# Kernel tuning notes

Measured on AMD Instinct MI355X. Metric: run time of the kernel, lower is better.

## Reference

```python
import jax, jax.numpy as jnp
import numpy as np

B, L, D = 128, 196, 1024  # batch, att_size, rnn_size


def setup_inputs() -> dict:
    key = jax.random.key(0)
    ks = jax.random.split(key, 11)
    s = 1.0 / np.sqrt(D)
    return {
        "x": jax.random.normal(ks[0], (B, D), jnp.float32),
        "att": jax.random.normal(ks[1], (B, L, D), jnp.float32),
        "h": jax.random.normal(ks[2], (B, D), jnp.float32),
        "W_a2a": jax.random.uniform(ks[3], (D, D), jnp.float32, -s, s),
        "b_a2a": jax.random.uniform(ks[4], (D,), jnp.float32, -s, s),
        "W_h2a": jax.random.uniform(ks[5], (D, D), jnp.float32, -s, s),
        "b_h2a": jax.random.uniform(ks[6], (D,), jnp.float32, -s, s),
        "W_i2a": jax.random.uniform(ks[7], (D, D), jnp.float32, -s, s),
        "b_i2a": jax.random.uniform(ks[8], (D,), jnp.float32, -s, s),
        "W_d2d": jax.random.uniform(ks[9], (D,), jnp.float32, -s, s),
        "b_d2d": jax.random.uniform(ks[10], (), jnp.float32, -s, s),
    }


def reference(x, att, h, W_a2a, b_a2a, W_h2a, b_h2a, W_i2a, b_i2a, W_d2d, b_d2d):
    # att_v_1: [B, L, D]
    att_v = jnp.einsum('bld,ed->ble', att, W_a2a) + b_a2a
    att_h = (h @ W_h2a.T + b_h2a)[:, None, :]   # [B, 1, D]
    att_x = (x @ W_i2a.T + b_i2a)[:, None, :]   # [B, 1, D]
    dot = jnp.tanh(att_v + att_h + att_x)       # [B, L, D]
    scores = jnp.einsum('bld,d->bl', dot, W_d2d) + b_d2d  # [B, L]
    weight = jax.nn.softmax(scores, axis=-1)    # [B, L]
    att_res = jnp.einsum('bld,bl->bd', att, weight)  # [B, D]
    return att_res
```

## Files before the change

kernel.cpp:

```cpp
#include <hip/hip_runtime.h>
#include <hip/hip_bf16.h>

#define B_ 128
#define L_ 196
#define D_ 1024

typedef __attribute__((ext_vector_type(8))) short short8v;
typedef __attribute__((ext_vector_type(4))) float f32x4;
typedef unsigned short ushort_t;

#define OFF_ATTBF   0UL
#define OFF_WBF     51380224UL
#define OFF_A2      53477376UL
#define OFF_W2      54001664UL
#define OFF_SPART   53477376UL
#define OFF_CPART   58195968UL

__device__ inline unsigned short f2bf(float f) {
  unsigned int u = __float_as_uint(f);
  unsigned int r = (u + 0x7fffu + ((u >> 16) & 1u)) >> 16;
  return (unsigned short)r;
}

__global__ void convert_kernel(const float* __restrict__ att, const float* __restrict__ Wa,
                               const float* __restrict__ x,   const float* __restrict__ h,
                               const float* __restrict__ Wi,  const float* __restrict__ Wh,
                               ushort_t* __restrict__ att_bf, ushort_t* __restrict__ W_bf,
                               ushort_t* __restrict__ A2,     ushort_t* __restrict__ W2) {
  const int n0 = (B_*L_*D_)/4;
  const int n1 = (D_*D_)/4;
  const int n2 = (B_*D_)/4;
  const int total = n0 + n1 + 2*n2 + 2*n1;
  for (int idx = blockIdx.x*blockDim.x + threadIdx.x; idx < total;
       idx += gridDim.x*blockDim.x) {
    const float4* src; ushort_t* dst;
    int i = idx;
    if (i < n0)               { src = (const float4*)att + i; dst = att_bf + (size_t)i*4; }
    else if ((i -= n0) < n1)  { src = (const float4*)Wa  + i; dst = W_bf  + (size_t)i*4; }
    else if ((i -= n1) < n2)  { int b = i>>8, k4 = i&255; src = (const float4*)x  + i; dst = A2 + b*2048 + k4*4; }
    else if ((i -= n2) < n2)  { int b = i>>8, k4 = i&255; src = (const float4*)h  + i; dst = A2 + b*2048 + 1024 + k4*4; }
    else if ((i -= n2) < n1)  { int e = i>>8, k4 = i&255; src = (const float4*)Wi + i; dst = W2 + e*2048 + k4*4; }
    else { i -= n1;             int e = i>>8, k4 = i&255; src = (const float4*)Wh + i; dst = W2 + e*2048 + 1024 + k4*4; }
    float4 v = *src;
    ushort4 o; o.x = f2bf(v.x); o.y = f2bf(v.y); o.z = f2bf(v.z); o.w = f2bf(v.w);
    *(ushort4*)dst = o;
  }
}

__device__ inline void stage_tile(const ushort_t* __restrict__ g, int row0, int Kld, int k0,
                                  ushort_t* ldst, int t) {
  #pragma unroll
  for (int it = 0; it < 4; ++it) {
    int linear = it*4096 + t*16;
    int r = linear >> 7;
    int c = (t & 7) ^ (r & 7);
    const ushort_t* src = g + (size_t)(row0 + r)*Kld + k0 + c*8;
    ushort_t* dst = ldst + ((it*4096 + ((t & 192) << 4)) >> 1);
    __builtin_amdgcn_global_load_lds((const __attribute__((address_space(1))) void*)src,
                                     (__attribute__((address_space(3))) void*)dst,
                                     16, 0, 0);
  }
}

__device__ inline short8v ldfrag(const ushort_t* tile, int row, int c) {
  int phys = c ^ (row & 7);
  return *(const short8v*)(tile + row*64 + phys*8);
}

__global__ __launch_bounds__(256) void gemm_c_kernel(
    const ushort_t* __restrict__ Amat, const ushort_t* __restrict__ Bmat,
    float* __restrict__ cpart) {
  __shared__ ushort_t lds[32768];
  int bid = blockIdx.x;
  int e0 = (bid & 7)*128;
  int kc = bid >> 3;
  int kbeg = kc*512;
  const int Kld = 2048;
  int t = threadIdx.x, lane = t & 63, w = t >> 6;
  int wm = w >> 1, we = w & 1;
  int lrow = lane & 15;
  int lk = lane >> 4;

  f32x4 acc[4][4];
  #pragma unroll
  for (int i = 0; i < 4; ++i)
    #pragma unroll
    for (int j = 0; j < 4; ++j) acc[i][j] = (f32x4){0.f, 0.f, 0.f, 0.f};

  stage_tile(Amat, 0,  Kld, kbeg, lds, t);
  stage_tile(Bmat, e0, Kld, kbeg, lds + 8192, t);
  __syncthreads();

  const int nk = 8;
  for (int kt = 0; kt < nk; ++kt) {
    int cur = kt & 1;
    if (kt + 1 < nk) {
      stage_tile(Amat, 0,  Kld, kbeg + ((kt+1) << 6), lds + (cur^1)*16384, t);
      stage_tile(Bmat, e0, Kld, kbeg + ((kt+1) << 6), lds + (cur^1)*16384 + 8192, t);
    }
    const ushort_t* At = lds + cur*16384;
    const ushort_t* Bt = At + 8192;
    #pragma unroll
    for (int hh = 0; hh < 2; ++hh) {
      short8v af[4], bfv[4];
      #pragma unroll
      for (int i = 0; i < 4; ++i) af[i]  = ldfrag(At, wm*64 + i*16 + lrow, hh*4 + lk);
      #pragma unroll
      for (int j = 0; j < 4; ++j) bfv[j] = ldfrag(Bt, we*64 + j*16 + lrow, hh*4 + lk);
      #pragma unroll
      for (int i = 0; i < 4; ++i)
        #pragma unroll
        for (int j = 0; j < 4; ++j)
          acc[i][j] = __builtin_amdgcn_mfma_f32_16x16x32_bf16(af[i], bfv[j], acc[i][j], 0, 0, 0);
    }
    __syncthreads();
  }

  float* outc = cpart + (size_t)kc*131072;
  #pragma unroll
  for (int i = 0; i < 4; ++i) {
    int m = wm*64 + i*16 + lk*4;
    #pragma unroll
    for (int j = 0; j < 4; ++j) {
      int e = e0 + we*64 + j*16 + lrow;
      #pragma unroll
      for (int r = 0; r < 4; ++r)
        outc[(m + r)*1024 + e] = acc[i][j][r];
    }
  }
}

#define BARR()  __builtin_amdgcn_s_barrier()
#define VM0()   asm volatile("s_waitcnt vmcnt(0)" ::: "memory")

__device__ inline void stageS(const ushort_t* __restrict__ g, int k0, ushort_t* ldsbase, int t) {
  #pragma unroll
  for (int it = 0; it < 4; ++it) {
    int linear = it*4096 + t*16;
    int r = linear >> 7;
    int c = ((linear >> 4) & 7) ^ (r & 7);
    const ushort_t* src = g + (size_t)r*1024 + k0 + c*8;
    ushort_t* dst = ldsbase + ((it*4096 + ((t & 192) << 4)) >> 1);
    __builtin_amdgcn_global_load_lds((const __attribute__((address_space(1))) void*)src,
                                     (__attribute__((address_space(3))) void*)dst,
                                     16, 0, 0);
  }
}

__global__ __launch_bounds__(256) void gemm_score_kernel(
    const ushort_t* __restrict__ Amat, const ushort_t* __restrict__ Bmat,
    const float* __restrict__ cpart,
    const float* __restrict__ ba, const float* __restrict__ bh, const float* __restrict__ bi,
    const float* __restrict__ wd,
    float* __restrict__ spart) {
  __shared__ ushort_t lds[16384];
  __shared__ float c_lds[256];
  int bid = blockIdx.x;
  int swz = (bid & 7)*196 + (bid >> 3);
  int m_blk = swz >> 3, n_blk = swz & 7;
  int m0 = m_blk*128, e0 = n_blk*128;
  int t = (int)threadIdx.x, lane = t & 63, w = t >> 6;
  int wm = w >> 1, we = w & 1;
  int lrow = lane & 15, lk = lane >> 4;

  int bb0 = m0 / 196;
  {
    int bb = bb0 + (t >> 7);
    int e  = e0 + (t & 127);
    float v = ba[e] + bh[e] + bi[e];
    if (bb < 128) {
      v += cpart[bb*1024 + e] + cpart[131072 + bb*1024 + e]
         + cpart[262144 + bb*1024 + e] + cpart[393216 + bb*1024 + e];
    }
    c_lds[t] = v;
  }

  const ushort_t* aG = Amat + (size_t)m0*1024;
  const ushort_t* bG = Bmat + (size_t)e0*1024;

  int lrow7 = lrow & 7;
  const ushort_t* pA0 = lds + (wm*64 + lrow)*64 + ((lk)     ^ lrow7)*8;
  const ushort_t* pA1 = lds + (wm*64 + lrow)*64 + (((4+lk)) ^ lrow7)*8;
  const ushort_t* pB0 = lds + 8192 + (we*64 + lrow)*64 + ((lk)     ^ lrow7)*8;
  const ushort_t* pB1 = lds + 8192 + (we*64 + lrow)*64 + (((4+lk)) ^ lrow7)*8;

  f32x4 acc[4][4];
  #pragma unroll
  for (int i = 0; i < 4; ++i)
    #pragma unroll
    for (int j = 0; j < 4; ++j) acc[i][j] = (f32x4){0.f, 0.f, 0.f, 0.f};

  stageS(aG, 0, lds, t);
  stageS(bG, 0, lds + 8192, t);

  for (int kt = 0; kt < 16; ++kt) {
    VM0();
    BARR();
    __builtin_amdgcn_s_setprio(1);
    #pragma unroll
    for (int ks = 0; ks < 2; ++ks) {
      const ushort_t* pa = ks ? pA1 : pA0;
      const ushort_t* pb = ks ? pB1 : pB0;
      short8v af[4], bfv[4];
      #pragma unroll
      for (int i = 0; i < 4; ++i) af[i]  = *(const short8v*)(pa + i*1024);
      #pragma unroll
      for (int j = 0; j < 4; ++j) bfv[j] = *(const short8v*)(pb + j*1024);
      #pragma unroll
      for (int i = 0; i < 4; ++i)
        #pragma unroll
        for (int j = 0; j < 4; ++j)
          acc[i][j] = __builtin_amdgcn_mfma_f32_16x16x32_bf16(af[i], bfv[j], acc[i][j], 0, 0, 0);
    }
    __builtin_amdgcn_s_setprio(0);
    BARR();
    if (kt < 15) {
      stageS(aG, (kt+1)*64, lds, t);
      stageS(bG, (kt+1)*64, lds + 8192, t);
    }
  }

  int p = n_blk*2 + we;
  #pragma unroll
  for (int i = 0; i < 4; ++i) {
    int mbase = m0 + wm*64 + i*16 + lk*4;
    f32x4 ps;
    #pragma unroll
    for (int r = 0; r < 4; ++r) {
      int m = mbase + r;
      int bb = (int)((unsigned)m / 196u);
      float partial = 0.f;
      #pragma unroll
      for (int j = 0; j < 4; ++j) {
        int ee = we*64 + j*16 + lrow;
        float v = acc[i][j][r] + c_lds[(bb - bb0)*128 + ee];
        float ex = __expf(2.f*v);
        partial += (1.f - 2.f/(ex + 1.f)) * wd[e0 + ee];
      }
      partial += __shfl_xor(partial, 1);
      partial += __shfl_xor(partial, 2);
      partial += __shfl_xor(partial, 4);
      partial += __shfl_xor(partial, 8);
      ps[r] = partial;
    }
    if (lrow == 0) *(f32x4*)(spart + (size_t)p*25088 + mbase) = ps;
  }
}

__global__ __launch_bounds__(256) void finalize_kernel(const ushort_t* __restrict__ att_bf,
                                                       const float* __restrict__ spart,
                                                       float* __restrict__ out) {
  int b  = blockIdx.x >> 1;
  int dh = blockIdx.x & 1;
  int t  = threadIdx.x;
  __shared__ float wls[L_];
  __shared__ float red[8];

  float s = -1e30f;
  if (t < L_) {
    int m = b*L_ + t;
    float sum = 0.f;
    #pragma unroll
    for (int p = 0; p < 16; ++p) sum += spart[p*25088 + m];
    s = sum;
  }
  float mx = s;
  #pragma unroll
  for (int off = 1; off < 64; off <<= 1) mx = fmaxf(mx, __shfl_xor(mx, off));
  if ((t & 63) == 0) red[t >> 6] = mx;
  __syncthreads();
  mx = fmaxf(fmaxf(red[0], red[1]), fmaxf(red[2], red[3]));
  float pr = (t < L_) ? __expf(s - mx) : 0.f;
  float ssum = pr;
  #pragma unroll
  for (int off = 1; off < 64; off <<= 1) ssum += __shfl_xor(ssum, off);
  if ((t & 63) == 0) red[4 + (t >> 6)] = ssum;
  __syncthreads();
  float tot = red[4] + red[5] + red[6] + red[7];
  if (t < L_) wls[t] = pr / tot;
  __syncthreads();

  int d = dh*512 + t*2;
  const ushort_t* abase = att_bf + (size_t)b*L_*D_ + d;
  float a0 = 0.f, a1 = 0.f;
  #pragma unroll 4
  for (int l = 0; l < L_; ++l) {
    float wv = wls[l];
    unsigned int v = *(const unsigned int*)(abase + (size_t)l*D_);
    float lo = __uint_as_float(v << 16);
    float hi = __uint_as_float(v & 0xffff0000u);
    a0 += wv*lo; a1 += wv*hi;
  }
  float2 o; o.x = a0; o.y = a1;
  *(float2*)(out + (size_t)b*D_ + d) = o;
}

extern "C" void kernel_launch(void* const* d_in, const int* in_sizes, int n_in,
                              void* d_out, int out_size, void* d_ws, size_t ws_size,
                              hipStream_t stream) {
  (void)in_sizes; (void)n_in; (void)out_size; (void)ws_size;
  const float* x   = (const float*)d_in[0];
  const float* att = (const float*)d_in[1];
  const float* h   = (const float*)d_in[2];
  const float* Wa  = (const float*)d_in[3];
  const float* ba  = (const float*)d_in[4];
  const float* Wh  = (const float*)d_in[5];
  const float* bh  = (const float*)d_in[6];
  const float* Wi  = (const float*)d_in[7];
  const float* bi  = (const float*)d_in[8];
  const float* wd  = (const float*)d_in[9];

  char* ws = (char*)d_ws;
  ushort_t* att_bf = (ushort_t*)(ws + OFF_ATTBF);
  ushort_t* W_bf   = (ushort_t*)(ws + OFF_WBF);
  ushort_t* A2     = (ushort_t*)(ws + OFF_A2);
  ushort_t* W2     = (ushort_t*)(ws + OFF_W2);
  float*    cpart  = (float*)(ws + OFF_CPART);
  float*    spart  = (float*)(ws + OFF_SPART);
  float*    out    = (float*)d_out;

  hipLaunchKernelGGL(convert_kernel, dim3(2048), dim3(256), 0, stream,
                     att, Wa, x, h, Wi, Wh, att_bf, W_bf, A2, W2);
  hipLaunchKernelGGL(gemm_c_kernel, dim3(32), dim3(256), 0, stream,
                     A2, W2, cpart);
  hipLaunchKernelGGL(gemm_score_kernel, dim3(1568), dim3(256), 0, stream,
                     att_bf, W_bf, cpart, ba, bh, bi, wd, spart);
  hipLaunchKernelGGL(finalize_kernel, dim3(256), dim3(256), 0, stream,
                     att_bf, spart, out);
}
```

Baseline: 127.7 us.

## Switch score GEMM to 32x32x16 MFMA and split finalize over more blocks

Replaces the 16x16x32 bf16 MFMA tiling in the score GEMM with 32x32x16 MFMAs on 2x2 accumulator tiles per wave. This cuts LDS fragment loads per MFMA and uses the larger instruction, and the tanh/score epilogue is remapped to the 32x32 output layout with a wider shuffle reduction. Separately, the finalize kernel now uses four blocks per batch with 128 active threads each, adding parallelism in the weighted-sum phase but leaving half the threads idle and recomputing the softmax twice as often. The new epilogue does scalar stores per row instead of vector stores.

```diff
diff --git a/kernel.cpp b/kernel.cpp
--- a/kernel.cpp
+++ b/kernel.cpp
@@ -7,6 +7,7 @@
 
 typedef __attribute__((ext_vector_type(8))) short short8v;
 typedef __attribute__((ext_vector_type(4))) float f32x4;
+typedef __attribute__((ext_vector_type(16))) float f32x16;
 typedef unsigned short ushort_t;
 
 #define OFF_ATTBF   0UL
@@ -161,7 +162,7 @@
   int m0 = m_blk*128, e0 = n_blk*128;
   int t = (int)threadIdx.x, lane = t & 63, w = t >> 6;
   int wm = w >> 1, we = w & 1;
-  int lrow = lane & 15, lk = lane >> 4;
+  int l31 = lane & 31, hi = lane >> 5, l7 = lane & 7;
 
   int bb0 = m0 / 196;
   {
@@ -178,17 +179,18 @@
   const ushort_t* aG = Amat + (size_t)m0*1024;
   const ushort_t* bG = Bmat + (size_t)e0*1024;
 
-  int lrow7 = lrow & 7;
-  const ushort_t* pA0 = lds + (wm*64 + lrow)*64 + ((lk)     ^ lrow7)*8;
-  const ushort_t* pA1 = lds + (wm*64 + lrow)*64 + (((4+lk)) ^ lrow7)*8;
-  const ushort_t* pB0 = lds + 8192 + (we*64 + lrow)*64 + ((lk)     ^ lrow7)*8;
-  const ushort_t* pB1 = lds + 8192 + (we*64 + lrow)*64 + (((4+lk)) ^ lrow7)*8;
-
-  f32x4 acc[4][4];
-  #pragma unroll
-  for (int i = 0; i < 4; ++i)
-    #pragma unroll
-    for (int j = 0; j < 4; ++j) acc[i][j] = (f32x4){0.f, 0.f, 0.f, 0.f};
+  const ushort_t* pA0 = lds + (wm*64 + l31)*64;
+  const ushort_t* pA1 = pA0 + 2048;
+  const ushort_t* pB0 = lds + 8192 + (we*64 + l31)*64;
+  const ushort_t* pB1 = pB0 + 2048;
+
+  f32x16 acc[2][2];
+  #pragma unroll
+  for (int i = 0; i < 2; ++i)
+    #pragma unroll
+    for (int j = 0; j < 2; ++j)
+      #pragma unroll
+      for (int r = 0; r < 16; ++r) acc[i][j][r] = 0.f;
 
   stageS(aG, 0, lds, t);
   stageS(bG, 0, lds + 8192, t);
@@ -198,19 +200,16 @@
     BARR();
     __builtin_amdgcn_s_setprio(1);
     #pragma unroll
-    for (int ks = 0; ks < 2; ++ks) {
-      const ushort_t* pa = ks ? pA1 : pA0;
-      const ushort_t* pb = ks ? pB1 : pB0;
-      short8v af[4], bfv[4];
-      #pragma unroll
-      for (int i = 0; i < 4; ++i) af[i]  = *(const short8v*)(pa + i*1024);
-      #pragma unroll
-      for (int j = 0; j < 4; ++j) bfv[j] = *(const short8v*)(pb + j*1024);
-      #pragma unroll
-      for (int i = 0; i < 4; ++i)
-        #pragma unroll
-        for (int j = 0; j < 4; ++j)
-          acc[i][j] = __builtin_amdgcn_mfma_f32_16x16x32_bf16(af[i], bfv[j], acc[i][j], 0, 0, 0);
+    for (int ks = 0; ks < 4; ++ks) {
+      int off = (((ks*2 + hi) ^ l7) * 8);
+      short8v a0 = *(const short8v*)(pA0 + off);
+      short8v a1 = *(const short8v*)(pA1 + off);
+      short8v b0 = *(const short8v*)(pB0 + off);
+      short8v b1 = *(const short8v*)(pB1 + off);
+      acc[0][0] = __builtin_amdgcn_mfma_f32_32x32x16_bf16(a0, b0, acc[0][0], 0, 0, 0);
+      acc[0][1] = __builtin_amdgcn_mfma_f32_32x32x16_bf16(a0, b1, acc[0][1], 0, 0, 0);
+      acc[1][0] = __builtin_amdgcn_mfma_f32_32x32x16_bf16(a1, b0, acc[1][0], 0, 0, 0);
+      acc[1][1] = __builtin_amdgcn_mfma_f32_32x32x16_bf16(a1, b1, acc[1][1], 0, 0, 0);
     }
     __builtin_amdgcn_s_setprio(0);
     BARR();
@@ -222,36 +221,34 @@
 
   int p = n_blk*2 + we;
   #pragma unroll
-  for (int i = 0; i < 4; ++i) {
-    int mbase = m0 + wm*64 + i*16 + lk*4;
-    f32x4 ps;
-    #pragma unroll
-    for (int r = 0; r < 4; ++r) {
-      int m = mbase + r;
+  for (int i = 0; i < 2; ++i) {
+    #pragma unroll
+    for (int reg = 0; reg < 16; ++reg) {
+      int m = m0 + wm*64 + i*32 + (reg&3) + 8*(reg>>2) + 4*hi;
       int bb = (int)((unsigned)m / 196u);
-      float partial = 0.f;
-      #pragma unroll
-      for (int j = 0; j < 4; ++j) {
-        int ee = we*64 + j*16 + lrow;
-        float v = acc[i][j][r] + c_lds[(bb - bb0)*128 + ee];
+      float s = 0.f;
+      #pragma unroll
+      for (int j = 0; j < 2; ++j) {
+        int ee = we*64 + j*32 + l31;
+        float v = acc[i][j][reg] + c_lds[(bb - bb0)*128 + ee];
         float ex = __expf(2.f*v);
-        partial += (1.f - 2.f/(ex + 1.f)) * wd[e0 + ee];
+        s += (1.f - 2.f/(ex + 1.f)) * wd[e0 + ee];
       }
-      partial += __shfl_xor(partial, 1);
-      partial += __shfl_xor(partial, 2);
-      partial += __shfl_xor(partial, 4);
-      partial += __shfl_xor(partial, 8);
-      ps[r] = partial;
-    }
-    if (lrow == 0) *(f32x4*)(spart + (size_t)p*25088 + mbase) = ps;
+      s += __shfl_xor(s, 1);
+      s += __shfl_xor(s, 2);
+      s += __shfl_xor(s, 4);
+      s += __shfl_xor(s, 8);
+      s += __shfl_xor(s, 16);
+      if (l31 == 0) spart[(size_t)p*25088 + m] = s;
+    }
   }
 }
 
 __global__ __launch_bounds__(256) void finalize_kernel(const ushort_t* __restrict__ att_bf,
                                                        const float* __restrict__ spart,
                                                        float* __restrict__ out) {
-  int b  = blockIdx.x >> 1;
-  int dh = blockIdx.x & 1;
+  int b  = blockIdx.x >> 2;
+  int dq = blockIdx.x & 3;
   int t  = threadIdx.x;
   __shared__ float wls[L_];
   __shared__ float red[8];
@@ -280,19 +277,21 @@
   if (t < L_) wls[t] = pr / tot;
   __syncthreads();
 
-  int d = dh*512 + t*2;
-  const ushort_t* abase = att_bf + (size_t)b*L_*D_ + d;
-  float a0 = 0.f, a1 = 0.f;
-  #pragma unroll 4
-  for (int l = 0; l < L_; ++l) {
-    float wv = wls[l];
-    unsigned int v = *(const unsigned int*)(abase + (size_t)l*D_);
-    float lo = __uint_as_float(v << 16);
-    float hi = __uint_as_float(v & 0xffff0000u);
-    a0 += wv*lo; a1 += wv*hi;
-  }
-  float2 o; o.x = a0; o.y = a1;
-  *(float2*)(out + (size_t)b*D_ + d) = o;
+  if (t < 128) {
+    int d = dq*256 + t*2;
+    const ushort_t* abase = att_bf + (size_t)b*L_*D_ + d;
+    float a0 = 0.f, a1 = 0.f;
+    #pragma unroll 4
+    for (int l = 0; l < L_; ++l) {
+      float wv = wls[l];
+      unsigned int v = *(const unsigned int*)(abase + (size_t)l*D_);
+      float lo = __uint_as_float(v << 16);
+      float hif = __uint_as_float(v & 0xffff0000u);
+      a0 += wv*lo; a1 += wv*hif;
+    }
+    float2 o; o.x = a0; o.y = a1;
+    *(float2*)(out + (size_t)b*D_ + d) = o;
+  }
 }
 
 extern "C" void kernel_launch(void* const* d_in, const int* in_sizes, int n_in,
@@ -325,6 +324,6 @@
                      A2, W2, cpart);
   hipLaunchKernelGGL(gemm_score_kernel, dim3(1568), dim3(256), 0, stream,
                      att_bf, W_bf, cpart, ba, bh, bi, wd, spart);
-  hipLaunchKernelGGL(finalize_kernel, dim3(256), dim3(256), 0, stream,
+  hipLaunchKernelGGL(finalize_kernel, dim3(512), dim3(256), 0, stream,
                      att_bf, spart, out);
 }
```

Measured after the change: 148.8 us. 1.17x slower.

## Make score GEMM persistent with next-tile prefetch; split finalize over quarters

Applied to the files above, without the earlier changes.

The score GEMM now runs as a persistent grid of 768 blocks, each looping over the 1568 tiles. The first K-slice of the next tile is prefetched during the last K-step of the current one, which hides part of the per-tile prologue latency. The finalize kernel is split into four D-quarters per batch row instead of two, giving more blocks for the bandwidth-bound weighted sum. The cost is that only half the threads in each finalize block do the sum, and the softmax work is repeated in every block. With a 768-block grid, tiles are spread unevenly: some blocks get three tiles and others two, which adds tail imbalance.

```diff
diff --git a/kernel.cpp b/kernel.cpp
--- a/kernel.cpp
+++ b/kernel.cpp
@@ -155,28 +155,10 @@
     float* __restrict__ spart) {
   __shared__ ushort_t lds[16384];
   __shared__ float c_lds[256];
-  int bid = blockIdx.x;
-  int swz = (bid & 7)*196 + (bid >> 3);
-  int m_blk = swz >> 3, n_blk = swz & 7;
-  int m0 = m_blk*128, e0 = n_blk*128;
+  const int NT = 1568, GRID = 768;
   int t = (int)threadIdx.x, lane = t & 63, w = t >> 6;
   int wm = w >> 1, we = w & 1;
   int lrow = lane & 15, lk = lane >> 4;
-
-  int bb0 = m0 / 196;
-  {
-    int bb = bb0 + (t >> 7);
-    int e  = e0 + (t & 127);
-    float v = ba[e] + bh[e] + bi[e];
-    if (bb < 128) {
-      v += cpart[bb*1024 + e] + cpart[131072 + bb*1024 + e]
-         + cpart[262144 + bb*1024 + e] + cpart[393216 + bb*1024 + e];
-    }
-    c_lds[t] = v;
-  }
-
-  const ushort_t* aG = Amat + (size_t)m0*1024;
-  const ushort_t* bG = Bmat + (size_t)e0*1024;
 
   int lrow7 = lrow & 7;
   const ushort_t* pA0 = lds + (wm*64 + lrow)*64 + ((lk)     ^ lrow7)*8;
@@ -184,74 +166,105 @@
   const ushort_t* pB0 = lds + 8192 + (we*64 + lrow)*64 + ((lk)     ^ lrow7)*8;
   const ushort_t* pB1 = lds + 8192 + (we*64 + lrow)*64 + (((4+lk)) ^ lrow7)*8;
 
-  f32x4 acc[4][4];
-  #pragma unroll
-  for (int i = 0; i < 4; ++i)
-    #pragma unroll
-    for (int j = 0; j < 4; ++j) acc[i][j] = (f32x4){0.f, 0.f, 0.f, 0.f};
-
-  stageS(aG, 0, lds, t);
-  stageS(bG, 0, lds + 8192, t);
-
-  for (int kt = 0; kt < 16; ++kt) {
-    VM0();
-    BARR();
-    __builtin_amdgcn_s_setprio(1);
-    #pragma unroll
-    for (int ks = 0; ks < 2; ++ks) {
-      const ushort_t* pa = ks ? pA1 : pA0;
-      const ushort_t* pb = ks ? pB1 : pB0;
-      short8v af[4], bfv[4];
-      #pragma unroll
-      for (int i = 0; i < 4; ++i) af[i]  = *(const short8v*)(pa + i*1024);
-      #pragma unroll
-      for (int j = 0; j < 4; ++j) bfv[j] = *(const short8v*)(pb + j*1024);
-      #pragma unroll
-      for (int i = 0; i < 4; ++i)
-        #pragma unroll
-        for (int j = 0; j < 4; ++j)
-          acc[i][j] = __builtin_amdgcn_mfma_f32_16x16x32_bf16(af[i], bfv[j], acc[i][j], 0, 0, 0);
-    }
-    __builtin_amdgcn_s_setprio(0);
-    BARR();
-    if (kt < 15) {
-      stageS(aG, (kt+1)*64, lds, t);
-      stageS(bG, (kt+1)*64, lds + 8192, t);
-    }
-  }
-
-  int p = n_blk*2 + we;
-  #pragma unroll
-  for (int i = 0; i < 4; ++i) {
-    int mbase = m0 + wm*64 + i*16 + lk*4;
-    f32x4 ps;
-    #pragma unroll
-    for (int r = 0; r < 4; ++r) {
-      int m = mbase + r;
-      int bb = (int)((unsigned)m / 196u);
-      float partial = 0.f;
-      #pragma unroll
-      for (int j = 0; j < 4; ++j) {
-        int ee = we*64 + j*16 + lrow;
-        float v = acc[i][j][r] + c_lds[(bb - bb0)*128 + ee];
-        float ex = __expf(2.f*v);
-        partial += (1.f - 2.f/(ex + 1.f)) * wd[e0 + ee];
+  {
+    int tid0 = blockIdx.x;
+    int swz0 = (tid0 & 7)*196 + (tid0 >> 3);
+    stageS(Amat + (size_t)(swz0 >> 3)*131072, 0, lds, t);
+    stageS(Bmat + (size_t)(swz0 & 7)*131072, 0, lds + 8192, t);
+  }
+
+  for (int tid = blockIdx.x; tid < NT; tid += GRID) {
+    int swz = (tid & 7)*196 + (tid >> 3);
+    int m_blk = swz >> 3, n_blk = swz & 7;
+    int m0 = m_blk*128, e0 = n_blk*128;
+    int bb0 = m0 / 196;
+
+    __syncthreads();
+    {
+      int bb = bb0 + (t >> 7);
+      int e  = e0 + (t & 127);
+      float v = ba[e] + bh[e] + bi[e];
+      if (bb < 128) {
+        v += cpart[bb*1024 + e] + cpart[131072 + bb*1024 + e]
+           + cpart[262144 + bb*1024 + e] + cpart[393216 + bb*1024 + e];
       }
-      partial += __shfl_xor(partial, 1);
-      partial += __shfl_xor(partial, 2);
-      partial += __shfl_xor(partial, 4);
-      partial += __shfl_xor(partial, 8);
-      ps[r] = partial;
-    }
-    if (lrow == 0) *(f32x4*)(spart + (size_t)p*25088 + mbase) = ps;
+      c_lds[t] = v;
+    }
+
+    const ushort_t* aG = Amat + (size_t)m0*1024;
+    const ushort_t* bG = Bmat + (size_t)e0*1024;
+
+    f32x4 acc[4][4];
+    #pragma unroll
+    for (int i = 0; i < 4; ++i)
+      #pragma unroll
+      for (int j = 0; j < 4; ++j) acc[i][j] = (f32x4){0.f, 0.f, 0.f, 0.f};
+
+    for (int kt = 0; kt < 16; ++kt) {
+      VM0();
+      BARR();
+      __builtin_amdgcn_s_setprio(1);
+      #pragma unroll
+      for (int ks = 0; ks < 2; ++ks) {
+        const ushort_t* pa = ks ? pA1 : pA0;
+        const ushort_t* pb = ks ? pB1 : pB0;
+        short8v af[4], bfv[4];
+        #pragma unroll
+        for (int i = 0; i < 4; ++i) af[i]  = *(const short8v*)(pa + i*1024);
+        #pragma unroll
+        for (int j = 0; j < 4; ++j) bfv[j] = *(const short8v*)(pb + j*1024);
+        #pragma unroll
+        for (int i = 0; i < 4; ++i)
+          #pragma unroll
+          for (int j = 0; j < 4; ++j)
+            acc[i][j] = __builtin_amdgcn_mfma_f32_16x16x32_bf16(af[i], bfv[j], acc[i][j], 0, 0, 0);
+      }
+      __builtin_amdgcn_s_setprio(0);
+      BARR();
+      if (kt < 15) {
+        stageS(aG, (kt+1)*64, lds, t);
+        stageS(bG, (kt+1)*64, lds + 8192, t);
+      } else if (tid + GRID < NT) {
+        int nt2 = tid + GRID;
+        int sz2 = (nt2 & 7)*196 + (nt2 >> 3);
+        stageS(Amat + (size_t)(sz2 >> 3)*131072, 0, lds, t);
+        stageS(Bmat + (size_t)(sz2 & 7)*131072, 0, lds + 8192, t);
+      }
+    }
+
+    int p = n_blk*2 + we;
+    #pragma unroll
+    for (int i = 0; i < 4; ++i) {
+      int mbase = m0 + wm*64 + i*16 + lk*4;
+      f32x4 ps;
+      #pragma unroll
+      for (int r = 0; r < 4; ++r) {
+        int m = mbase + r;
+        int bb = (int)((unsigned)m / 196u);
+        float partial = 0.f;
+        #pragma unroll
+        for (int j = 0; j < 4; ++j) {
+          int ee = we*64 + j*16 + lrow;
+          float v = acc[i][j][r] + c_lds[(bb - bb0)*128 + ee];
+          float ex = __expf(2.f*v);
+          partial += (1.f - 2.f/(ex + 1.f)) * wd[e0 + ee];
+        }
+        partial += __shfl_xor(partial, 1);
+        partial += __shfl_xor(partial, 2);
+        partial += __shfl_xor(partial, 4);
+        partial += __shfl_xor(partial, 8);
+        ps[r] = partial;
+      }
+      if (lrow == 0) *(f32x4*)(spart + (size_t)p*25088 + mbase) = ps;
+    }
   }
 }
 
 __global__ __launch_bounds__(256) void finalize_kernel(const ushort_t* __restrict__ att_bf,
                                                        const float* __restrict__ spart,
                                                        float* __restrict__ out) {
-  int b  = blockIdx.x >> 1;
-  int dh = blockIdx.x & 1;
+  int b  = blockIdx.x >> 2;
+  int dq = blockIdx.x & 3;
   int t  = threadIdx.x;
   __shared__ float wls[L_];
   __shared__ float red[8];
@@ -280,19 +293,21 @@
   if (t < L_) wls[t] = pr / tot;
   __syncthreads();
 
-  int d = dh*512 + t*2;
-  const ushort_t* abase = att_bf + (size_t)b*L_*D_ + d;
-  float a0 = 0.f, a1 = 0.f;
-  #pragma unroll 4
-  for (int l = 0; l < L_; ++l) {
-    float wv = wls[l];
-    unsigned int v = *(const unsigned int*)(abase + (size_t)l*D_);
-    float lo = __uint_as_float(v << 16);
-    float hi = __uint_as_float(v & 0xffff0000u);
-    a0 += wv*lo; a1 += wv*hi;
-  }
-  float2 o; o.x = a0; o.y = a1;
-  *(float2*)(out + (size_t)b*D_ + d) = o;
+  if (t < 128) {
+    int d = dq*256 + t*2;
+    const ushort_t* abase = att_bf + (size_t)b*L_*D_ + d;
+    float a0 = 0.f, a1 = 0.f;
+    #pragma unroll 4
+    for (int l = 0; l < L_; ++l) {
+      float wv = wls[l];
+      unsigned int v = *(const unsigned int*)(abase + (size_t)l*D_);
+      float lo = __uint_as_float(v << 16);
+      float hif = __uint_as_float(v & 0xffff0000u);
+      a0 += wv*lo; a1 += wv*hif;
+    }
+    float2 o; o.x = a0; o.y = a1;
+    *(float2*)(out + (size_t)b*D_ + d) = o;
+  }
 }
 
 extern "C" void kernel_launch(void* const* d_in, const int* in_sizes, int n_in,
@@ -323,8 +338,8 @@
                      att, Wa, x, h, Wi, Wh, att_bf, W_bf, A2, W2);
   hipLaunchKernelGGL(gemm_c_kernel, dim3(32), dim3(256), 0, stream,
                      A2, W2, cpart);
-  hipLaunchKernelGGL(gemm_score_kernel, dim3(1568), dim3(256), 0, stream,
+  hipLaunchKernelGGL(gemm_score_kernel, dim3(768), dim3(256), 0, stream,
                      att_bf, W_bf, cpart, ba, bh, bi, wd, spart);
-  hipLaunchKernelGGL(finalize_kernel, dim3(256), dim3(256), 0, stream,
+  hipLaunchKernelGGL(finalize_kernel, dim3(512), dim3(256), 0, stream,
                      att_bf, spart, out);
 }
```

Result: slower. 149.4 us (+17.0%).

## Fuse att fp32-to-bf16 conversion into GEMM A-tile load path

Applied to the files above, without the earlier changes.

Removes the separate pass that converts the whole att tensor to bf16 in the workspace. The score GEMM now loads fp32 att directly into registers, packs it with v_cvt_pk_bf16_f32 and writes it to LDS, prefetching the next k-tile while MFMAs run. Finalize reads fp32 att directly and is split into quarter-D blocks. This saves the write and re-read of a large bf16 copy, at the cost of doubled A-tile global traffic inside the GEMM (8 GEMM column blocks each reread fp32 att) and register pressure.

```diff
diff --git a/kernel.cpp b/kernel.cpp
--- a/kernel.cpp
+++ b/kernel.cpp
@@ -9,12 +9,11 @@
 typedef __attribute__((ext_vector_type(4))) float f32x4;
 typedef unsigned short ushort_t;
 
-#define OFF_ATTBF   0UL
-#define OFF_WBF     51380224UL
-#define OFF_A2      53477376UL
-#define OFF_W2      54001664UL
-#define OFF_SPART   53477376UL
-#define OFF_CPART   58195968UL
+#define OFF_WBF     0UL
+#define OFF_A2      2097152UL
+#define OFF_W2      2621440UL
+#define OFF_SPART   6815744UL
+#define OFF_CPART   8421376UL
 
 __device__ inline unsigned short f2bf(float f) {
   unsigned int u = __float_as_uint(f);
@@ -22,21 +21,25 @@
   return (unsigned short)r;
 }
 
-__global__ void convert_kernel(const float* __restrict__ att, const float* __restrict__ Wa,
+__device__ inline unsigned int pk2(float a, float b) {
+  unsigned int r;
+  asm volatile("v_cvt_pk_bf16_f32 %0, %1, %2" : "=v"(r) : "v"(a), "v"(b));
+  return r;
+}
+
+__global__ void convert_kernel(const float* __restrict__ Wa,
                                const float* __restrict__ x,   const float* __restrict__ h,
                                const float* __restrict__ Wi,  const float* __restrict__ Wh,
-                               ushort_t* __restrict__ att_bf, ushort_t* __restrict__ W_bf,
+                               ushort_t* __restrict__ W_bf,
                                ushort_t* __restrict__ A2,     ushort_t* __restrict__ W2) {
-  const int n0 = (B_*L_*D_)/4;
   const int n1 = (D_*D_)/4;
   const int n2 = (B_*D_)/4;
-  const int total = n0 + n1 + 2*n2 + 2*n1;
+  const int total = n1 + 2*n2 + 2*n1;
   for (int idx = blockIdx.x*blockDim.x + threadIdx.x; idx < total;
        idx += gridDim.x*blockDim.x) {
     const float4* src; ushort_t* dst;
     int i = idx;
-    if (i < n0)               { src = (const float4*)att + i; dst = att_bf + (size_t)i*4; }
-    else if ((i -= n0) < n1)  { src = (const float4*)Wa  + i; dst = W_bf  + (size_t)i*4; }
+    if (i < n1)               { src = (const float4*)Wa  + i; dst = W_bf + (size_t)i*4; }
     else if ((i -= n1) < n2)  { int b = i>>8, k4 = i&255; src = (const float4*)x  + i; dst = A2 + b*2048 + k4*4; }
     else if ((i -= n2) < n2)  { int b = i>>8, k4 = i&255; src = (const float4*)h  + i; dst = A2 + b*2048 + 1024 + k4*4; }
     else if ((i -= n2) < n1)  { int e = i>>8, k4 = i&255; src = (const float4*)Wi + i; dst = W2 + e*2048 + k4*4; }
@@ -132,6 +135,9 @@
 
 #define BARR()  __builtin_amdgcn_s_barrier()
 #define VM0()   asm volatile("s_waitcnt vmcnt(0)" ::: "memory")
+#define VM8()   asm volatile("s_waitcnt vmcnt(8)" ::: "memory")
+#define VM4()   asm volatile("s_waitcnt vmcnt(4)" ::: "memory")
+#define LGKM0() asm volatile("s_waitcnt lgkmcnt(0)" ::: "memory")
 
 __device__ inline void stageS(const ushort_t* __restrict__ g, int k0, ushort_t* ldsbase, int t) {
   #pragma unroll
@@ -148,7 +154,7 @@
 }
 
 __global__ __launch_bounds__(256) void gemm_score_kernel(
-    const ushort_t* __restrict__ Amat, const ushort_t* __restrict__ Bmat,
+    const float* __restrict__ attf, const ushort_t* __restrict__ Bmat,
     const float* __restrict__ cpart,
     const float* __restrict__ ba, const float* __restrict__ bh, const float* __restrict__ bi,
     const float* __restrict__ wd,
@@ -175,8 +181,11 @@
     c_lds[t] = v;
   }
 
-  const ushort_t* aG = Amat + (size_t)m0*1024;
   const ushort_t* bG = Bmat + (size_t)e0*1024;
+
+  int ar = t >> 3, ac = t & 7;
+  const float* ald = attf + (size_t)(m0 + ar)*1024 + ac*8;
+  ushort_t* awr = lds + ar*64 + ((ac ^ (ar & 7))*8);
 
   int lrow7 = lrow & 7;
   const ushort_t* pA0 = lds + (wm*64 + lrow)*64 + ((lk)     ^ lrow7)*8;
@@ -190,11 +199,38 @@
     #pragma unroll
     for (int j = 0; j < 4; ++j) acc[i][j] = (f32x4){0.f, 0.f, 0.f, 0.f};
 
-  stageS(aG, 0, lds, t);
   stageS(bG, 0, lds + 8192, t);
+  float4 La[4][2];
+  #pragma unroll
+  for (int it = 0; it < 4; ++it) {
+    La[it][0] = *(const float4*)(ald + (size_t)it*32768);
+    La[it][1] = *(const float4*)(ald + (size_t)it*32768 + 4);
+  }
+  VM0();
+  uint4 Aw[4];
+  #pragma unroll
+  for (int it = 0; it < 4; ++it) {
+    Aw[it].x = pk2(La[it][0].x, La[it][0].y);
+    Aw[it].y = pk2(La[it][0].z, La[it][0].w);
+    Aw[it].z = pk2(La[it][1].x, La[it][1].y);
+    Aw[it].w = pk2(La[it][1].z, La[it][1].w);
+  }
 
   for (int kt = 0; kt < 16; ++kt) {
-    VM0();
+    #pragma unroll
+    for (int it = 0; it < 4; ++it)
+      *reinterpret_cast<uint4*>(awr + it*2048) = Aw[it];
+    if (kt < 15) {
+      #pragma unroll
+      for (int it = 0; it < 4; ++it) {
+        La[it][0] = *(const float4*)(ald + (size_t)it*32768 + (kt+1)*64);
+        La[it][1] = *(const float4*)(ald + (size_t)it*32768 + (kt+1)*64 + 4);
+      }
+      VM8();
+    } else {
+      VM0();
+    }
+    LGKM0();
     BARR();
     __builtin_amdgcn_s_setprio(1);
     #pragma unroll
@@ -215,8 +251,15 @@
     __builtin_amdgcn_s_setprio(0);
     BARR();
     if (kt < 15) {
-      stageS(aG, (kt+1)*64, lds, t);
       stageS(bG, (kt+1)*64, lds + 8192, t);
+      VM4();
+      #pragma unroll
+      for (int it = 0; it < 4; ++it) {
+        Aw[it].x = pk2(La[it][0].x, La[it][0].y);
+        Aw[it].y = pk2(La[it][0].z, La[it][0].w);
+        Aw[it].z = pk2(La[it][1].x, La[it][1].y);
+        Aw[it].w = pk2(La[it][1].z, La[it][1].w);
+      }
     }
   }
 
@@ -247,11 +290,11 @@
   }
 }
 
-__global__ __launch_bounds__(256) void finalize_kernel(const ushort_t* __restrict__ att_bf,
+__global__ __launch_bounds__(256) void finalize_kernel(const float* __restrict__ att,
                                                        const float* __restrict__ spart,
                                                        float* __restrict__ out) {
-  int b  = blockIdx.x >> 1;
-  int dh = blockIdx.x & 1;
+  int b  = blockIdx.x >> 2;
+  int dq = blockIdx.x & 3;
   int t  = threadIdx.x;
   __shared__ float wls[L_];
   __shared__ float red[8];
@@ -280,19 +323,19 @@
   if (t < L_) wls[t] = pr / tot;
   __syncthreads();
 
-  int d = dh*512 + t*2;
-  const ushort_t* abase = att_bf + (size_t)b*L_*D_ + d;
-  float a0 = 0.f, a1 = 0.f;
-  #pragma unroll 4
-  for (int l = 0; l < L_; ++l) {
-    float wv = wls[l];
-    unsigned int v = *(const unsigned int*)(abase + (size_t)l*D_);
-    float lo = __uint_as_float(v << 16);
-    float hi = __uint_as_float(v & 0xffff0000u);
-    a0 += wv*lo; a1 += wv*hi;
-  }
-  float2 o; o.x = a0; o.y = a1;
-  *(float2*)(out + (size_t)b*D_ + d) = o;
+  if (t < 128) {
+    int d = dq*256 + t*2;
+    const float* abase = att + (size_t)b*L_*D_ + d;
+    float a0 = 0.f, a1 = 0.f;
+    #pragma unroll 4
+    for (int l = 0; l < L_; ++l) {
+      float wv = wls[l];
+      float2 av = *(const float2*)(abase + (size_t)l*D_);
+      a0 += wv*av.x; a1 += wv*av.y;
+    }
+    float2 o; o.x = a0; o.y = a1;
+    *(float2*)(out + (size_t)b*D_ + d) = o;
+  }
 }
 
 extern "C" void kernel_launch(void* const* d_in, const int* in_sizes, int n_in,
@@ -311,20 +354,19 @@
   const float* wd  = (const float*)d_in[9];
 
   char* ws = (char*)d_ws;
-  ushort_t* att_bf = (ushort_t*)(ws + OFF_ATTBF);
   ushort_t* W_bf   = (ushort_t*)(ws + OFF_WBF);
   ushort_t* A2     = (ushort_t*)(ws + OFF_A2);
   ushort_t* W2     = (ushort_t*)(ws + OFF_W2);
+  float*    spart  = (float*)(ws + OFF_SPART);
   float*    cpart  = (float*)(ws + OFF_CPART);
-  float*    spart  = (float*)(ws + OFF_SPART);
   float*    out    = (float*)d_out;
 
-  hipLaunchKernelGGL(convert_kernel, dim3(2048), dim3(256), 0, stream,
-                     att, Wa, x, h, Wi, Wh, att_bf, W_bf, A2, W2);
+  hipLaunchKernelGGL(convert_kernel, dim3(1024), dim3(256), 0, stream,
+                     Wa, x, h, Wi, Wh, W_bf, A2, W2);
   hipLaunchKernelGGL(gemm_c_kernel, dim3(32), dim3(256), 0, stream,
                      A2, W2, cpart);
   hipLaunchKernelGGL(gemm_score_kernel, dim3(1568), dim3(256), 0, stream,
-                     att_bf, W_bf, cpart, ba, bh, bi, wd, spart);
-  hipLaunchKernelGGL(finalize_kernel, dim3(256), dim3(256), 0, stream,
-                     att_bf, spart, out);
-}
+                     att, W_bf, cpart, ba, bh, bi, wd, spart);
+  hipLaunchKernelGGL(finalize_kernel, dim3(512), dim3(256), 0, stream,
+                     att, spart, out);
+}
```

After: 133.9 us. 4.8% more time.
